# Performance work log

Measured on AMD Instinct MI355X. Metric: run time of the kernel, lower is better.

Reference implementation:

```python
import jax, jax.numpy as jnp
import numpy as np

SHAPES = [(100, 100), (50, 50), (25, 25), (13, 13)]
N_HEADS, N_LEVELS, N_POINTS, D_MODEL, D_FFN = 8, 4, 4, 256, 1024
HEAD_DIM = D_MODEL // N_HEADS
S_TOTAL = sum(h * w for h, w in SHAPES)
BATCH = 2


def _layernorm(x, g, b, eps=1e-5):
    m = jnp.mean(x, -1, keepdims=True)
    v = jnp.mean((x - m) ** 2, -1, keepdims=True)
    return (x - m) * jax.lax.rsqrt(v + eps) * g + b


def _bilinear_sample(value_l, loc, Hl, Wl):
    # value_l: (N, Hl, Wl, nh, hd); loc: (N, Lq, nh, P, 2) normalized to [0,1]
    # Matches torch grid_sample(mode='bilinear', padding_mode='zeros', align_corners=False)
    x = loc[..., 0] * Wl - 0.5
    y = loc[..., 1] * Hl - 0.5
    x0 = jnp.floor(x); y0 = jnp.floor(y)
    wx1 = x - x0; wx0 = 1.0 - wx1
    wy1 = y - y0; wy0 = 1.0 - wy1
    x0i = x0.astype(jnp.int32); x1i = x0i + 1
    y0i = y0.astype(jnp.int32); y1i = y0i + 1
    N, Lq, nh, P = x.shape
    n_idx = jnp.arange(N)[:, None, None, None]
    h_idx = jnp.arange(nh)[None, None, :, None]

    def gather(yi, xi):
        valid = (yi >= 0) & (yi < Hl) & (xi >= 0) & (xi < Wl)
        yc = jnp.clip(yi, 0, Hl - 1); xc = jnp.clip(xi, 0, Wl - 1)
        v = value_l[n_idx, yc, xc, h_idx]  # (N, Lq, nh, P, hd)
        return v * valid[..., None].astype(v.dtype)

    return (gather(y0i, x0i) * (wy0 * wx0)[..., None]
            + gather(y0i, x1i) * (wy0 * wx1)[..., None]
            + gather(y1i, x0i) * (wy1 * wx0)[..., None]
            + gather(y1i, x1i) * (wy1 * wx1)[..., None])


def _forward(src, pos, reference_points, W_off, b_off, W_attn, b_attn, W_val, b_val,
             W_out, b_out, W1, b1, W2, b2, g1, beta1, g2, beta2):
    N, S, C = src.shape
    q = src + pos  # with_pos_embed
    # MSDeformAttn
    off = (q @ W_off + b_off).reshape(N, S, N_HEADS, N_LEVELS, N_POINTS, 2)
    aw = jax.nn.softmax((q @ W_attn + b_attn).reshape(N, S, N_HEADS, N_LEVELS * N_POINTS), axis=-1)
    aw = aw.reshape(N, S, N_HEADS, N_LEVELS, N_POINTS)
    value = (src @ W_val + b_val).reshape(N, S, N_HEADS, HEAD_DIM)
    # offset normalizer is (W_l, H_l) per level
    normalizer = jnp.array([[wl, hl] for hl, wl in SHAPES], dtype=src.dtype)  # (L, 2)
    loc = reference_points[:, :, None, :, None, :] + off / normalizer[None, None, None, :, None, :]
    out = jnp.zeros((N, S, N_HEADS, HEAD_DIM), src.dtype)
    start = 0
    for l, (Hl, Wl) in enumerate(SHAPES):
        v_l = value[:, start:start + Hl * Wl].reshape(N, Hl, Wl, N_HEADS, HEAD_DIM)
        sampled = _bilinear_sample(v_l, loc[:, :, :, l], Hl, Wl)  # (N,S,nh,P,hd)
        out = out + jnp.einsum('nqhp,nqhpd->nqhd', aw[:, :, :, l], sampled)
        start += Hl * Wl
    src2 = out.reshape(N, S, C) @ W_out + b_out
    # residual + norm1 (dropout is identity in eval)
    x = _layernorm(src + src2, g1, beta1)
    # FFN + residual + norm2
    ff = jax.nn.relu(x @ W1 + b1) @ W2 + b2
    return _layernorm(x + ff, g2, beta2)


def setup_inputs() -> dict:
    key = jax.random.key(0)
    ks = jax.random.split(key, 16)
    f32 = jnp.float32

    def w(k, shape, scale=0.02):
        return jax.random.normal(k, shape, dtype=f32) * scale

    return {
        "src": jax.random.normal(ks[0], (BATCH, S_TOTAL, D_MODEL), dtype=f32),
        "pos": jax.random.normal(ks[1], (BATCH, S_TOTAL, D_MODEL), dtype=f32),
        "reference_points": jax.random.uniform(ks[2], (BATCH, S_TOTAL, N_LEVELS, 2), dtype=f32),
        "spatial_shapes": jnp.array(SHAPES, dtype=jnp.int32),
        "level_start_index": jnp.array(np.cumsum([0] + [h * w for h, w in SHAPES[:-1]]), dtype=jnp.int32),
        "W_off": w(ks[3], (D_MODEL, N_HEADS * N_LEVELS * N_POINTS * 2)),
        "b_off": w(ks[4], (N_HEADS * N_LEVELS * N_POINTS * 2,), 0.5),
        "W_attn": w(ks[5], (D_MODEL, N_HEADS * N_LEVELS * N_POINTS)),
        "b_attn": w(ks[6], (N_HEADS * N_LEVELS * N_POINTS,)),
        "W_val": w(ks[7], (D_MODEL, D_MODEL)),
        "b_val": w(ks[8], (D_MODEL,)),
        "W_out": w(ks[9], (D_MODEL, D_MODEL)),
        "b_out": w(ks[10], (D_MODEL,)),
        "W1": w(ks[11], (D_MODEL, D_FFN)),
        "b1": w(ks[12], (D_FFN,)),
        "W2": w(ks[13], (D_FFN, D_MODEL)),
        "b2": w(ks[14], (D_MODEL,)),
        "g1": jnp.ones((D_MODEL,), f32),
        "beta1": jnp.zeros((D_MODEL,), f32),
        "g2": jnp.ones((D_MODEL,), f32),
        "beta2": jnp.zeros((D_MODEL,), f32),
    }


def reference(src, pos, reference_points, spatial_shapes, level_start_index,
              W_off, b_off, W_attn, b_attn, W_val, b_val, W_out, b_out,
              W1, b1, W2, b2, g1, beta1, g2, beta2):
    # spatial_shapes / level_start_index are static metadata mirrored by SHAPES
    return _forward(src, pos, reference_points, W_off, b_off, W_attn, b_attn,
                    W_val, b_val, W_out, b_out, W1, b1, W2, b2, g1, beta1, g2, beta2)
```

## Files before the change

kernel.cpp:

```cpp
#include <hip/hip_runtime.h>


typedef __bf16 bf16x8 __attribute__((ext_vector_type(8)));
typedef __bf16 bf16x4 __attribute__((ext_vector_type(4)));
typedef float floatx4 __attribute__((ext_vector_type(4)));

#define S_TOTAL 13294
#define M_ROWS  26588
#define M_PAD   26624
#define DMODEL  256

struct CvtArgs {
    const float *Woff, *Wattn, *Wval, *Wout, *W1, *W2, *boff, *battn;
};
__global__ __launch_bounds__(256) void cvt_all(CvtArgs a, __bf16* __restrict__ wdst,
                                               float* __restrict__ bc) {
    int i = blockIdx.x * 256 + threadIdx.x;
    if (i < 65536) {
        wdst[i] = (__bf16)a.Woff[(i & 255) * 256 + (i >> 8)];
    } else if (i < 98304) {
        int j = i - 65536;
        wdst[i] = (__bf16)a.Wattn[(j & 255) * 128 + (j >> 8)];
    } else if (i < 163840) {
        int j = i - 98304;
        wdst[i] = (__bf16)a.Wval[(j & 255) * 256 + (j >> 8)];
    } else if (i < 229376) {
        int j = i - 163840;
        wdst[i] = (__bf16)a.Wout[(j & 255) * 256 + (j >> 8)];
    } else if (i < 491520) {
        int j = i - 229376;
        wdst[i] = (__bf16)a.W1[(j & 255) * 1024 + (j >> 8)];
    } else if (i < 753664) {
        int j = i - 491520;
        wdst[i] = (__bf16)a.W2[(j & 1023) * 256 + (j >> 10)];
    } else if (i < 754048) {
        int j = i - 753664;
        bc[j] = (j < 256) ? a.boff[j] : a.battn[j - 256];
    }
}

__global__ __launch_bounds__(256) void prep_k(const float* __restrict__ src,
                                              const float* __restrict__ pos,
                                              __bf16* __restrict__ qb,
                                              __bf16* __restrict__ srcb) {
    int i4 = blockIdx.x * 256 + threadIdx.x;
    size_t e = (size_t)i4 * 4;
    if (e < (size_t)M_ROWS * DMODEL) {
        float4 s = *(const float4*)(src + e);
        float4 p = *(const float4*)(pos + e);
        bf16x4 q = {(__bf16)(s.x + p.x), (__bf16)(s.y + p.y),
                    (__bf16)(s.z + p.z), (__bf16)(s.w + p.w)};
        bf16x4 sb = {(__bf16)s.x, (__bf16)s.y, (__bf16)s.z, (__bf16)s.w};
        *(bf16x4*)(qb + e)   = q;
        *(bf16x4*)(srcb + e) = sb;
    } else {
        bf16x4 z = {(__bf16)0.f, (__bf16)0.f, (__bf16)0.f, (__bf16)0.f};
        *(bf16x4*)(qb + e)   = z;
        *(bf16x4*)(srcb + e) = z;
    }
}

template <int BM, int KT, int J, bool RELU, bool BF16OUT, bool ACCUM>
__global__ __launch_bounds__(512, 4) void gemm_ares(const __bf16* __restrict__ A,
                                                    int lda,
                                                    const __bf16* __restrict__ BT,
                                                    int ldb,
                                                    const float* __restrict__ bias,
                                                    float* __restrict__ Cf,
                                                    __bf16* __restrict__ Cb,
                                                    int N) {
    constexpr int GPR = KT / 8;
    __shared__ __align__(16) __bf16 As[BM * KT];
    __shared__ __align__(16) float  patch[8][16 * 20];

    const int tid  = threadIdx.x;
    const int row0 = blockIdx.y * BM;
    const int wave = tid >> 6, lane = tid & 63;
    const int l16  = lane & 15, quad = lane >> 4;

#pragma unroll
    for (int it = 0; it < BM * GPR / 512; it++) {
        int fg = it * 512 + tid;
        int m  = fg / GPR, g = fg % GPR;
        bf16x8 v = *(const bf16x8*)(A + (size_t)(row0 + m) * lda + g * 8);
        *(bf16x8*)(As + m * KT + (g ^ (m & 31)) * 8) = v;
    }
    __syncthreads();

    const int n0 = blockIdx.x * (8 * J * 16) + wave * (J * 16);
    floatx4 acc[BM / 16][J] = {};

#pragma unroll 4
    for (int ki = 0; ki < KT / 32; ki++) {
        bf16x8 af[BM / 16], bfr[J];
#pragma unroll
        for (int i = 0; i < BM / 16; i++) {
            int row = i * 16 + l16;
            int g   = ki * 4 + quad;
            af[i] = *(const bf16x8*)(As + row * KT + (g ^ (row & 31)) * 8);
        }
#pragma unroll
        for (int j = 0; j < J; j++) {
            int n = n0 + j * 16 + l16;
            bfr[j] = *(const bf16x8*)(BT + (size_t)n * ldb + ki * 32 + quad * 8);
        }
#pragma unroll
        for (int i = 0; i < BM / 16; i++)
#pragma unroll
            for (int j = 0; j < J; j++)
                acc[i][j] = __builtin_amdgcn_mfma_f32_16x16x32_bf16(
                    af[i], bfr[j], acc[i][j], 0, 0, 0);
    }

    float bvj[J];
#pragma unroll
    for (int j = 0; j < J; j++) bvj[j] = bias ? bias[n0 + j * 16 + l16] : 0.f;

    float* pat = patch[wave];
    const int prow = lane >> 2, pc = lane & 3;
#pragma unroll
    for (int i = 0; i < BM / 16; i++)
#pragma unroll
        for (int j = 0; j < J; j++) {
#pragma unroll
            for (int r = 0; r < 4; r++) {
                float v = acc[i][j][r] + bvj[j];
                if (RELU) v = fmaxf(v, 0.f);
                pat[(quad * 4 + r) * 20 + l16] = v;
            }
            float4 v4 = *(float4*)&pat[prow * 20 + pc * 4];
            size_t gi = (size_t)(row0 + i * 16 + prow) * N + n0 + j * 16 + pc * 4;
            if (BF16OUT) {
                bf16x4 ob = {(__bf16)v4.x, (__bf16)v4.y, (__bf16)v4.z, (__bf16)v4.w};
                *(bf16x4*)(Cb + gi) = ob;
            } else if (ACCUM) {
                float4 c4 = *(const float4*)(Cf + gi);
                v4.x += c4.x; v4.y += c4.y; v4.z += c4.z; v4.w += c4.w;
                *(float4*)(Cf + gi) = v4;
            } else {
                *(float4*)(Cf + gi) = v4;
            }
        }
}

__global__ __launch_bounds__(256) void sample_k(const float* __restrict__ offa,
                                                const __bf16* __restrict__ valb,
                                                const float* __restrict__ refp,
                                                __bf16* __restrict__ outb) {
    const int r   = blockIdx.x;
    const int tid = threadIdx.x;
    if (r >= M_ROWS) {
        outb[(size_t)r * 256 + tid] = (__bf16)0.f;
        return;
    }
    __shared__ float2 s_wo[4][128];
    const int n = (r >= S_TOTAL) ? 1 : 0;

    if (tid < 128) {
        const int HLc[4] = {100, 50, 25, 13};
        const int STc[4] = {0, 10000, 12500, 13125};
        int lp = tid & 15, l = lp >> 2;
        float logit = offa[(size_t)r * 384 + 256 + tid];
        float mx = logit;
        mx = fmaxf(mx, __shfl_xor(mx, 1));
        mx = fmaxf(mx, __shfl_xor(mx, 2));
        mx = fmaxf(mx, __shfl_xor(mx, 4));
        mx = fmaxf(mx, __shfl_xor(mx, 8));
        float e = __expf(logit - mx);
        float s = e;
        s += __shfl_xor(s, 1); s += __shfl_xor(s, 2);
        s += __shfl_xor(s, 4); s += __shfl_xor(s, 8);
        float aw = e / s;

        float2 o2 = *(const float2*)(offa + (size_t)r * 384 + tid * 2);
        float rx = refp[((size_t)r * 4 + l) * 2];
        float ry = refp[((size_t)r * 4 + l) * 2 + 1];
        int   Wl = HLc[l];
        float x = rx * (float)Wl + o2.x - 0.5f;
        float y = ry * (float)Wl + o2.y - 0.5f;
        float xf = floorf(x), yf = floorf(y);
        float wx1 = x - xf, wy1 = y - yf;
        float wx0 = 1.f - wx1, wy0 = 1.f - wy1;
        int x0 = (int)xf, y0 = (int)yf;
        int base = n * S_TOTAL + STc[l];
#pragma unroll
        for (int c = 0; c < 4; c++) {
            int yy = y0 + (c >> 1), xx = x0 + (c & 1);
            bool valid = (yy >= 0) & (yy < Wl) & (xx >= 0) & (xx < Wl);
            int yc = min(max(yy, 0), Wl - 1);
            int xc = min(max(xx, 0), Wl - 1);
            float w = ((c >> 1) ? wy1 : wy0) * ((c & 1) ? wx1 : wx0);
            int off = (base + yc * Wl + xc) * 512;
            s_wo[c][tid] = make_float2(valid ? w * aw : 0.f, __int_as_float(off));
        }
    }
    __syncthreads();

    const int h  = tid >> 5;
    const int pg = (tid >> 2) & 7;
    const int cg = tid & 3;
    const char* vbase = (const char*)valb + h * 64 + cg * 16;
    float a[8] = {};
#pragma unroll
    for (int pp = 0; pp < 2; pp++) {
        int idx = h * 16 + pg * 2 + pp;
#pragma unroll
        for (int c = 0; c < 4; c++) {
            float2 wo = s_wo[c][idx];
            float  w  = wo.x;
            bf16x8 v  = *(const bf16x8*)(vbase + __float_as_int(wo.y));
#pragma unroll
            for (int k = 0; k < 8; k++) a[k] += w * (float)v[k];
        }
    }
#pragma unroll
    for (int k = 0; k < 8; k++) {
        a[k] += __shfl_xor(a[k], 4);
        a[k] += __shfl_xor(a[k], 8);
        a[k] += __shfl_xor(a[k], 16);
    }
    if (pg == 0) {
        bf16x8 res;
#pragma unroll
        for (int k = 0; k < 8; k++) res[k] = (__bf16)a[k];
        *(bf16x8*)(outb + (size_t)r * 256 + h * 32 + cg * 8) = res;
    }
}

__global__ __launch_bounds__(64) void ln1_k(const float* __restrict__ src,
                                            const float* __restrict__ src2,
                                            const float* __restrict__ g,
                                            const float* __restrict__ b,
                                            float* __restrict__ x,
                                            __bf16* __restrict__ xb) {
    const int r = blockIdx.x, lane = threadIdx.x;
    if (r >= M_ROWS) {
        bf16x4 z = {(__bf16)0.f, (__bf16)0.f, (__bf16)0.f, (__bf16)0.f};
        *(bf16x4*)(xb + (size_t)r * 256 + lane * 4) = z;
        return;
    }
    size_t base = (size_t)r * 256 + lane * 4;
    float4 a = *(const float4*)(src + base);
    float4 c = *(const float4*)(src2 + base);
    float v0 = a.x + c.x, v1 = a.y + c.y, v2 = a.z + c.z, v3 = a.w + c.w;
    float s  = v0 + v1 + v2 + v3;
    float sq = v0 * v0 + v1 * v1 + v2 * v2 + v3 * v3;
    for (int o = 32; o > 0; o >>= 1) {
        s  += __shfl_xor(s, o);
        sq += __shfl_xor(sq, o);
    }
    float mean = s * (1.f / 256.f);
    float var  = sq * (1.f / 256.f) - mean * mean;
    float rs   = rsqrtf(var + 1e-5f);
    float4 gg = *(const float4*)(g + lane * 4);
    float4 bb = *(const float4*)(b + lane * 4);
    float o0 = (v0 - mean) * rs * gg.x + bb.x;
    float o1 = (v1 - mean) * rs * gg.y + bb.y;
    float o2 = (v2 - mean) * rs * gg.z + bb.z;
    float o3 = (v3 - mean) * rs * gg.w + bb.w;
    *(float4*)(x + base) = make_float4(o0, o1, o2, o3);
    bf16x4 ob = {(__bf16)o0, (__bf16)o1, (__bf16)o2, (__bf16)o3};
    *(bf16x4*)(xb + base) = ob;
}

__global__ __launch_bounds__(64) void ln2_k(const float* __restrict__ t,
                                            const float* __restrict__ g,
                                            const float* __restrict__ b,
                                            float* __restrict__ out) {
    const int r = blockIdx.x, lane = threadIdx.x;
    size_t base = (size_t)r * 256 + lane * 4;
    float4 a = *(const float4*)(t + base);
    float v0 = a.x, v1 = a.y, v2 = a.z, v3 = a.w;
    float s  = v0 + v1 + v2 + v3;
    float sq = v0 * v0 + v1 * v1 + v2 * v2 + v3 * v3;
    for (int o = 32; o > 0; o >>= 1) {
        s  += __shfl_xor(s, o);
        sq += __shfl_xor(sq, o);
    }
    float mean = s * (1.f / 256.f);
    float var  = sq * (1.f / 256.f) - mean * mean;
    float rs   = rsqrtf(var + 1e-5f);
    float4 gg = *(const float4*)(g + lane * 4);
    float4 bb = *(const float4*)(b + lane * 4);
    float4 o4;
    o4.x = (v0 - mean) * rs * gg.x + bb.x;
    o4.y = (v1 - mean) * rs * gg.y + bb.y;
    o4.z = (v2 - mean) * rs * gg.z + bb.z;
    o4.w = (v3 - mean) * rs * gg.w + bb.w;
    *(float4*)(out + base) = o4;
}

extern "C" void kernel_launch(void* const* d_in, const int* in_sizes, int n_in,
                              void* d_out, int out_size, void* d_ws, size_t ws_size,
                              hipStream_t stream) {
    const float* src  = (const float*)d_in[0];
    const float* pos  = (const float*)d_in[1];
    const float* refp = (const float*)d_in[2];
    const float* W_off  = (const float*)d_in[5];
    const float* b_off  = (const float*)d_in[6];
    const float* W_attn = (const float*)d_in[7];
    const float* b_attn = (const float*)d_in[8];
    const float* W_val  = (const float*)d_in[9];
    const float* b_val  = (const float*)d_in[10];
    const float* W_out  = (const float*)d_in[11];
    const float* b_out  = (const float*)d_in[12];
    const float* W1     = (const float*)d_in[13];
    const float* b1     = (const float*)d_in[14];
    const float* W2     = (const float*)d_in[15];
    const float* b2     = (const float*)d_in[16];
    const float* g1     = (const float*)d_in[17];
    const float* beta1  = (const float*)d_in[18];
    const float* g2     = (const float*)d_in[19];
    const float* beta2  = (const float*)d_in[20];
    float* out = (float*)d_out;

    const size_t RB = (size_t)M_PAD * 256 * 2;
    const size_t RF = (size_t)M_PAD * 256 * 4;
    char* ws = (char*)d_ws;
    __bf16* qb   = (__bf16*)(ws);
    __bf16* srcb = (__bf16*)(ws + RB);
    float*  offa = (float*)(ws + 2 * RB);
    __bf16* valb = (__bf16*)(ws + 2 * RB + (size_t)M_PAD * 384 * 4);
    __bf16* outb = qb;
    float*  src2 = (float*)(ws + RB);
    float*  x    = (float*)(ws + RB + RF);
    __bf16* xb   = qb;
    __bf16* hbh  = (__bf16*)(ws + 2 * RB + (size_t)M_PAD * 384 * 4);
    char*   regW = ws + 2 * RB + (size_t)M_PAD * 384 * 4 + (size_t)M_PAD * 512 * 2;

    __bf16* WTcomb = (__bf16*)regW;
    __bf16* WTval  = (__bf16*)(regW + 196608);
    __bf16* WTout  = (__bf16*)(regW + 327680);
    __bf16* WT1    = (__bf16*)(regW + 458752);
    __bf16* WT2    = (__bf16*)(regW + 983040);
    float*  bc     = (float*)(regW + 1507328);

    CvtArgs ca = {W_off, W_attn, W_val, W_out, W1, W2, b_off, b_attn};
    cvt_all<<<(754048 + 255) / 256, 256, 0, stream>>>(ca, WTcomb, bc);

    prep_k<<<M_PAD * 256 / 4 / 256, 256, 0, stream>>>(src, pos, qb, srcb);

    gemm_ares<64, 256, 3, false, false, false><<<dim3(1, 416), 512, 0, stream>>>(
        qb, 256, WTcomb, 256, bc, offa, nullptr, 384);
    gemm_ares<64, 256, 2, false, true, false><<<dim3(1, 416), 512, 0, stream>>>(
        srcb, 256, WTval, 256, b_val, nullptr, valb, 256);

    sample_k<<<M_PAD, 256, 0, stream>>>(offa, valb, refp, outb);

    gemm_ares<64, 256, 2, false, false, false><<<dim3(1, 416), 512, 0, stream>>>(
        outb, 256, WTout, 256, b_out, src2, nullptr, 256);
    ln1_k<<<M_PAD, 64, 0, stream>>>(src, src2, g1, beta1, x, xb);

    for (int half = 0; half < 2; half++) {
        gemm_ares<64, 256, 2, true, true, false><<<dim3(2, 416), 512, 0, stream>>>(
            xb, 256, WT1 + (size_t)half * 512 * 256, 256, b1 + half * 512,
            nullptr, hbh, 512);
        gemm_ares<32, 512, 2, false, false, true><<<dim3(1, 832), 512, 0, stream>>>(
            hbh, 512, WT2 + half * 512, 1024, half == 0 ? b2 : nullptr,
            x, nullptr, 256);
    }
    ln2_k<<<M_ROWS, 64, 0, stream>>>(x, g2, beta2, out);
}
```

Measured before the change: 392.6 us.

## Fuse input prep into GEMMs, output proj with LN1, and full FFN with LN2

Replaces the separate prep, LayerNorm and split FFN kernels with fused kernels. The offset/value GEMMs now read fp32 src/pos directly and convert to bf16 in shared memory. The output projection folds in the residual add and LayerNorm1, and a single FFN kernel keeps the hidden activations in LDS before applying LayerNorm2. The weight-convert kernel now transposes through LDS tiles so its global accesses are coalesced. This removes several intermediate global round-trips and kernel launches, at the cost of more LDS per block and lower parallelism in the fused FFN.

```diff
diff --git a/kernel.cpp b/kernel.cpp
--- a/kernel.cpp
+++ b/kernel.cpp
@@ -8,135 +8,106 @@
 #define S_TOTAL 13294
 #define M_ROWS  26588
 #define M_PAD   26624
-#define DMODEL  256
-
-struct CvtArgs {
-    const float *Woff, *Wattn, *Wval, *Wout, *W1, *W2, *boff, *battn;
-};
-__global__ __launch_bounds__(256) void cvt_all(CvtArgs a, __bf16* __restrict__ wdst,
-                                               float* __restrict__ bc) {
-    int i = blockIdx.x * 256 + threadIdx.x;
-    if (i < 65536) {
-        wdst[i] = (__bf16)a.Woff[(i & 255) * 256 + (i >> 8)];
-    } else if (i < 98304) {
-        int j = i - 65536;
-        wdst[i] = (__bf16)a.Wattn[(j & 255) * 128 + (j >> 8)];
-    } else if (i < 163840) {
-        int j = i - 98304;
-        wdst[i] = (__bf16)a.Wval[(j & 255) * 256 + (j >> 8)];
-    } else if (i < 229376) {
-        int j = i - 163840;
-        wdst[i] = (__bf16)a.Wout[(j & 255) * 256 + (j >> 8)];
-    } else if (i < 491520) {
-        int j = i - 229376;
-        wdst[i] = (__bf16)a.W1[(j & 255) * 1024 + (j >> 8)];
-    } else if (i < 753664) {
-        int j = i - 491520;
-        wdst[i] = (__bf16)a.W2[(j & 1023) * 256 + (j >> 10)];
-    } else if (i < 754048) {
-        int j = i - 753664;
-        bc[j] = (j < 256) ? a.boff[j] : a.battn[j - 256];
-    }
-}
-
-__global__ __launch_bounds__(256) void prep_k(const float* __restrict__ src,
-                                              const float* __restrict__ pos,
-                                              __bf16* __restrict__ qb,
-                                              __bf16* __restrict__ srcb) {
-    int i4 = blockIdx.x * 256 + threadIdx.x;
-    size_t e = (size_t)i4 * 4;
-    if (e < (size_t)M_ROWS * DMODEL) {
-        float4 s = *(const float4*)(src + e);
-        float4 p = *(const float4*)(pos + e);
-        bf16x4 q = {(__bf16)(s.x + p.x), (__bf16)(s.y + p.y),
-                    (__bf16)(s.z + p.z), (__bf16)(s.w + p.w)};
-        bf16x4 sb = {(__bf16)s.x, (__bf16)s.y, (__bf16)s.z, (__bf16)s.w};
-        *(bf16x4*)(qb + e)   = q;
-        *(bf16x4*)(srcb + e) = sb;
-    } else {
-        bf16x4 z = {(__bf16)0.f, (__bf16)0.f, (__bf16)0.f, (__bf16)0.f};
-        *(bf16x4*)(qb + e)   = z;
-        *(bf16x4*)(srcb + e) = z;
-    }
-}
-
-template <int BM, int KT, int J, bool RELU, bool BF16OUT, bool ACCUM>
-__global__ __launch_bounds__(512, 4) void gemm_ares(const __bf16* __restrict__ A,
-                                                    int lda,
-                                                    const __bf16* __restrict__ BT,
-                                                    int ldb,
-                                                    const float* __restrict__ bias,
-                                                    float* __restrict__ Cf,
-                                                    __bf16* __restrict__ Cb,
-                                                    int N) {
-    constexpr int GPR = KT / 8;
-    __shared__ __align__(16) __bf16 As[BM * KT];
-    __shared__ __align__(16) float  patch[8][16 * 20];
-
-    const int tid  = threadIdx.x;
-    const int row0 = blockIdx.y * BM;
-    const int wave = tid >> 6, lane = tid & 63;
-    const int l16  = lane & 15, quad = lane >> 4;
-
-#pragma unroll
-    for (int it = 0; it < BM * GPR / 512; it++) {
-        int fg = it * 512 + tid;
-        int m  = fg / GPR, g = fg % GPR;
-        bf16x8 v = *(const bf16x8*)(A + (size_t)(row0 + m) * lda + g * 8);
-        *(bf16x8*)(As + m * KT + (g ^ (m & 31)) * 8) = v;
-    }
-    __syncthreads();
-
-    const int n0 = blockIdx.x * (8 * J * 16) + wave * (J * 16);
-    floatx4 acc[BM / 16][J] = {};
-
-#pragma unroll 4
-    for (int ki = 0; ki < KT / 32; ki++) {
-        bf16x8 af[BM / 16], bfr[J];
-#pragma unroll
-        for (int i = 0; i < BM / 16; i++) {
-            int row = i * 16 + l16;
-            int g   = ki * 4 + quad;
-            af[i] = *(const bf16x8*)(As + row * KT + (g ^ (row & 31)) * 8);
-        }
-#pragma unroll
-        for (int j = 0; j < J; j++) {
-            int n = n0 + j * 16 + l16;
-            bfr[j] = *(const bf16x8*)(BT + (size_t)n * ldb + ki * 32 + quad * 8);
-        }
-#pragma unroll
-        for (int i = 0; i < BM / 16; i++)
+
+#define MFMA16(a, b, c) __builtin_amdgcn_mfma_f32_16x16x32_bf16(a, b, c, 0, 0, 0)
+
+__global__ __launch_bounds__(256) void cvt_k(
+    const float* __restrict__ Woff, const float* __restrict__ Wattn,
+    const float* __restrict__ Wval, const float* __restrict__ Wout,
+    const float* __restrict__ W1,   const float* __restrict__ W2,
+    const float* __restrict__ boff, const float* __restrict__ battn,
+    __bf16* __restrict__ wbase, float* __restrict__ bc) {
+    int b = blockIdx.x;
+    if (b >= 184) {
+        for (int i = threadIdx.x; i < 384; i += 256)
+            bc[i] = (i < 256) ? boff[i] : battn[i - 256];
+        return;
+    }
+    const float* W; __bf16* D; int K, N, t;
+    if (b < 16)       { W = Woff;  D = wbase;          K = 256;  N = 256;  t = b; }
+    else if (b < 24)  { W = Wattn; D = wbase + 65536;  K = 256;  N = 128;  t = b - 16; }
+    else if (b < 40)  { W = Wval;  D = wbase + 98304;  K = 256;  N = 256;  t = b - 24; }
+    else if (b < 56)  { W = Wout;  D = wbase + 163840; K = 256;  N = 256;  t = b - 40; }
+    else if (b < 120) { W = W1;    D = wbase + 229376; K = 256;  N = 1024; t = b - 56; }
+    else              { W = W2;    D = wbase + 491520; K = 1024; N = 256;  t = b - 120; }
+    int tk = K >> 6;
+    int n0 = (t / tk) << 6, k0 = (t % tk) << 6;
+    __shared__ float T[64][65];
+    int tid = threadIdx.x;
+    int rr = tid >> 4, cc = (tid & 15) << 2;
+#pragma unroll
+    for (int p = 0; p < 4; p++) {
+        int r = p * 16 + rr;
+        float4 v = *(const float4*)(W + (size_t)(k0 + r) * N + n0 + cc);
+        T[r][cc] = v.x; T[r][cc + 1] = v.y; T[r][cc + 2] = v.z; T[r][cc + 3] = v.w;
+    }
+    __syncthreads();
+#pragma unroll
+    for (int p = 0; p < 4; p++) {
+        int n = p * 16 + rr;
+        bf16x4 o = {(__bf16)T[cc][n], (__bf16)T[cc + 1][n],
+                    (__bf16)T[cc + 2][n], (__bf16)T[cc + 3][n]};
+        *(bf16x4*)(D + (size_t)(n0 + n) * K + k0 + cc) = o;
+    }
+}
+
+template <int J, bool SUMPOS, bool BF16OUT>
+__global__ __launch_bounds__(512, 4) void gemm_src(
+    const float* __restrict__ Af, const float* __restrict__ Pf,
+    const __bf16* __restrict__ BT, const float* __restrict__ bias,
+    float* __restrict__ Cf, __bf16* __restrict__ Cb, int N) {
+    constexpr int ASTR = 264;
+    __shared__ __align__(16) __bf16 As[64 * ASTR];
+    __shared__ __align__(16) float patch[8][16 * 20];
+    const int tid = threadIdx.x, wave = tid >> 6, lane = tid & 63;
+    const int l16 = lane & 15, quad = lane >> 4;
+    const int row0 = blockIdx.x * 64;
+#pragma unroll
+    for (int p = 0; p < 8; p++) {
+        int fe = (p * 512 + tid) * 4;
+        int m = fe >> 8, k = fe & 255;
+        int row = min(row0 + m, M_ROWS - 1);
+        float4 s = *(const float4*)(Af + (size_t)row * 256 + k);
+        if (SUMPOS) {
+            float4 pp = *(const float4*)(Pf + (size_t)row * 256 + k);
+            s.x += pp.x; s.y += pp.y; s.z += pp.z; s.w += pp.w;
+        }
+        bf16x4 v = {(__bf16)s.x, (__bf16)s.y, (__bf16)s.z, (__bf16)s.w};
+        *(bf16x4*)(As + m * ASTR + k) = v;
+    }
+    __syncthreads();
+    const int n0 = wave * (J * 16);
+    floatx4 acc[4][J] = {};
+#pragma unroll
+    for (int ki = 0; ki < 8; ki++) {
+        bf16x8 af[4], bfr[J];
+#pragma unroll
+        for (int i = 0; i < 4; i++)
+            af[i] = *(const bf16x8*)(As + (i * 16 + l16) * ASTR + ki * 32 + quad * 8);
+#pragma unroll
+        for (int j = 0; j < J; j++)
+            bfr[j] = *(const bf16x8*)(BT + (size_t)(n0 + j * 16 + l16) * 256 + ki * 32 + quad * 8);
+#pragma unroll
+        for (int i = 0; i < 4; i++)
 #pragma unroll
             for (int j = 0; j < J; j++)
-                acc[i][j] = __builtin_amdgcn_mfma_f32_16x16x32_bf16(
-                    af[i], bfr[j], acc[i][j], 0, 0, 0);
-    }
-
-    float bvj[J];
-#pragma unroll
-    for (int j = 0; j < J; j++) bvj[j] = bias ? bias[n0 + j * 16 + l16] : 0.f;
-
+                acc[i][j] = MFMA16(af[i], bfr[j], acc[i][j]);
+    }
     float* pat = patch[wave];
     const int prow = lane >> 2, pc = lane & 3;
 #pragma unroll
-    for (int i = 0; i < BM / 16; i++)
+    for (int i = 0; i < 4; i++)
 #pragma unroll
         for (int j = 0; j < J; j++) {
-#pragma unroll
-            for (int r = 0; r < 4; r++) {
-                float v = acc[i][j][r] + bvj[j];
-                if (RELU) v = fmaxf(v, 0.f);
-                pat[(quad * 4 + r) * 20 + l16] = v;
-            }
+            float bv = bias[n0 + j * 16 + l16];
+#pragma unroll
+            for (int r = 0; r < 4; r++)
+                pat[(quad * 4 + r) * 20 + l16] = acc[i][j][r] + bv;
             float4 v4 = *(float4*)&pat[prow * 20 + pc * 4];
             size_t gi = (size_t)(row0 + i * 16 + prow) * N + n0 + j * 16 + pc * 4;
             if (BF16OUT) {
                 bf16x4 ob = {(__bf16)v4.x, (__bf16)v4.y, (__bf16)v4.z, (__bf16)v4.w};
                 *(bf16x4*)(Cb + gi) = ob;
-            } else if (ACCUM) {
-                float4 c4 = *(const float4*)(Cf + gi);
-                v4.x += c4.x; v4.y += c4.y; v4.z += c4.z; v4.w += c4.w;
-                *(float4*)(Cf + gi) = v4;
             } else {
                 *(float4*)(Cf + gi) = v4;
             }
@@ -227,67 +198,228 @@
     }
 }
 
-__global__ __launch_bounds__(64) void ln1_k(const float* __restrict__ src,
-                                            const float* __restrict__ src2,
-                                            const float* __restrict__ g,
-                                            const float* __restrict__ b,
-                                            float* __restrict__ x,
-                                            __bf16* __restrict__ xb) {
-    const int r = blockIdx.x, lane = threadIdx.x;
-    if (r >= M_ROWS) {
-        bf16x4 z = {(__bf16)0.f, (__bf16)0.f, (__bf16)0.f, (__bf16)0.f};
-        *(bf16x4*)(xb + (size_t)r * 256 + lane * 4) = z;
-        return;
-    }
-    size_t base = (size_t)r * 256 + lane * 4;
-    float4 a = *(const float4*)(src + base);
-    float4 c = *(const float4*)(src2 + base);
-    float v0 = a.x + c.x, v1 = a.y + c.y, v2 = a.z + c.z, v3 = a.w + c.w;
-    float s  = v0 + v1 + v2 + v3;
-    float sq = v0 * v0 + v1 * v1 + v2 * v2 + v3 * v3;
-    for (int o = 32; o > 0; o >>= 1) {
-        s  += __shfl_xor(s, o);
-        sq += __shfl_xor(sq, o);
-    }
-    float mean = s * (1.f / 256.f);
-    float var  = sq * (1.f / 256.f) - mean * mean;
-    float rs   = rsqrtf(var + 1e-5f);
-    float4 gg = *(const float4*)(g + lane * 4);
-    float4 bb = *(const float4*)(b + lane * 4);
-    float o0 = (v0 - mean) * rs * gg.x + bb.x;
-    float o1 = (v1 - mean) * rs * gg.y + bb.y;
-    float o2 = (v2 - mean) * rs * gg.z + bb.z;
-    float o3 = (v3 - mean) * rs * gg.w + bb.w;
-    *(float4*)(x + base) = make_float4(o0, o1, o2, o3);
-    bf16x4 ob = {(__bf16)o0, (__bf16)o1, (__bf16)o2, (__bf16)o3};
-    *(bf16x4*)(xb + base) = ob;
-}
-
-__global__ __launch_bounds__(64) void ln2_k(const float* __restrict__ t,
-                                            const float* __restrict__ g,
-                                            const float* __restrict__ b,
-                                            float* __restrict__ out) {
-    const int r = blockIdx.x, lane = threadIdx.x;
-    size_t base = (size_t)r * 256 + lane * 4;
-    float4 a = *(const float4*)(t + base);
-    float v0 = a.x, v1 = a.y, v2 = a.z, v3 = a.w;
-    float s  = v0 + v1 + v2 + v3;
-    float sq = v0 * v0 + v1 * v1 + v2 * v2 + v3 * v3;
-    for (int o = 32; o > 0; o >>= 1) {
-        s  += __shfl_xor(s, o);
-        sq += __shfl_xor(sq, o);
-    }
-    float mean = s * (1.f / 256.f);
-    float var  = sq * (1.f / 256.f) - mean * mean;
-    float rs   = rsqrtf(var + 1e-5f);
-    float4 gg = *(const float4*)(g + lane * 4);
-    float4 bb = *(const float4*)(b + lane * 4);
-    float4 o4;
-    o4.x = (v0 - mean) * rs * gg.x + bb.x;
-    o4.y = (v1 - mean) * rs * gg.y + bb.y;
-    o4.z = (v2 - mean) * rs * gg.z + bb.z;
-    o4.w = (v3 - mean) * rs * gg.w + bb.w;
-    *(float4*)(out + base) = o4;
+__global__ __launch_bounds__(512, 4) void oln_k(
+    const __bf16* __restrict__ A, const __bf16* __restrict__ BT,
+    const float* __restrict__ bias, const float* __restrict__ src,
+    const float* __restrict__ g, const float* __restrict__ be,
+    float* __restrict__ x, __bf16* __restrict__ xb) {
+    constexpr int ASTR = 264;
+    __shared__ __align__(16) __bf16 As[64 * ASTR];
+    __shared__ __align__(16) float patch[8][16 * 20];
+    __shared__ float2 rowred[64][9];
+    const int tid = threadIdx.x, wave = tid >> 6, lane = tid & 63;
+    const int l16 = lane & 15, quad = lane >> 4;
+    const int prow = lane >> 2, pc = lane & 3;
+    const int row0 = blockIdx.x * 64;
+#pragma unroll
+    for (int p = 0; p < 4; p++) {
+        int fg = p * 512 + tid;
+        int m = fg >> 5, gg = fg & 31;
+        bf16x8 v = *(const bf16x8*)(A + (size_t)(row0 + m) * 256 + gg * 8);
+        *(bf16x8*)(As + m * ASTR + gg * 8) = v;
+    }
+    __syncthreads();
+    const int n0 = wave * 32;
+    floatx4 acc[4][2] = {};
+#pragma unroll
+    for (int ki = 0; ki < 8; ki++) {
+        bf16x8 af[4], bfr[2];
+#pragma unroll
+        for (int i = 0; i < 4; i++)
+            af[i] = *(const bf16x8*)(As + (i * 16 + l16) * ASTR + ki * 32 + quad * 8);
+#pragma unroll
+        for (int j = 0; j < 2; j++)
+            bfr[j] = *(const bf16x8*)(BT + (size_t)(n0 + j * 16 + l16) * 256 + ki * 32 + quad * 8);
+#pragma unroll
+        for (int i = 0; i < 4; i++)
+#pragma unroll
+            for (int j = 0; j < 2; j++)
+                acc[i][j] = MFMA16(af[i], bfr[j], acc[i][j]);
+    }
+    float* pat = patch[wave];
+    floatx4 v4[4][2];
+#pragma unroll
+    for (int i = 0; i < 4; i++) {
+        int rowc = min(row0 + i * 16 + prow, M_ROWS - 1);
+        float s_par = 0.f, q_par = 0.f;
+#pragma unroll
+        for (int j = 0; j < 2; j++) {
+            float bv = bias[n0 + j * 16 + l16];
+#pragma unroll
+            for (int r = 0; r < 4; r++)
+                pat[(quad * 4 + r) * 20 + l16] = acc[i][j][r] + bv;
+            float4 t4 = *(float4*)&pat[prow * 20 + pc * 4];
+            float4 r4 = *(const float4*)(src + (size_t)rowc * 256 + n0 + j * 16 + pc * 4);
+            floatx4 w; w[0] = t4.x + r4.x; w[1] = t4.y + r4.y;
+            w[2] = t4.z + r4.z; w[3] = t4.w + r4.w;
+            v4[i][j] = w;
+            s_par += w[0] + w[1] + w[2] + w[3];
+            q_par += w[0] * w[0] + w[1] * w[1] + w[2] * w[2] + w[3] * w[3];
+        }
+        s_par += __shfl_xor(s_par, 1); s_par += __shfl_xor(s_par, 2);
+        q_par += __shfl_xor(q_par, 1); q_par += __shfl_xor(q_par, 2);
+        if (pc == 0) rowred[i * 16 + prow][wave] = make_float2(s_par, q_par);
+    }
+    __syncthreads();
+#pragma unroll
+    for (int i = 0; i < 4; i++) {
+        float ss = 0.f, qq = 0.f;
+#pragma unroll
+        for (int w8 = 0; w8 < 8; w8++) {
+            float2 t = rowred[i * 16 + prow][w8];
+            ss += t.x; qq += t.y;
+        }
+        float mean = ss * (1.f / 256.f);
+        float var  = qq * (1.f / 256.f) - mean * mean;
+        float rstd = rsqrtf(var + 1e-5f);
+#pragma unroll
+        for (int j = 0; j < 2; j++) {
+            int col = n0 + j * 16 + pc * 4;
+            float4 g4 = *(const float4*)(g + col);
+            float4 b4 = *(const float4*)(be + col);
+            floatx4 w = v4[i][j];
+            float4 o4;
+            o4.x = (w[0] - mean) * rstd * g4.x + b4.x;
+            o4.y = (w[1] - mean) * rstd * g4.y + b4.y;
+            o4.z = (w[2] - mean) * rstd * g4.z + b4.z;
+            o4.w = (w[3] - mean) * rstd * g4.w + b4.w;
+            size_t gi = (size_t)(row0 + i * 16 + prow) * 256 + col;
+            *(float4*)(x + gi) = o4;
+            bf16x4 ob = {(__bf16)o4.x, (__bf16)o4.y, (__bf16)o4.z, (__bf16)o4.w};
+            *(bf16x4*)(xb + gi) = ob;
+        }
+    }
+}
+
+__global__ __launch_bounds__(512, 4) void ffn_k(
+    const __bf16* __restrict__ xb, const __bf16* __restrict__ W1T,
+    const __bf16* __restrict__ W2T, const float* __restrict__ b1,
+    const float* __restrict__ b2, const float* __restrict__ x,
+    const float* __restrict__ g, const float* __restrict__ be,
+    float* __restrict__ out) {
+    constexpr int ASTR = 264, HSTR = 520;
+    __shared__ __align__(16) __bf16 As[32 * ASTR];
+    __shared__ __align__(16) __bf16 Hs[32 * HSTR];
+    __shared__ __align__(16) float patch[8][16 * 20];
+    __shared__ float2 rowred[32][9];
+    const int tid = threadIdx.x, wave = tid >> 6, lane = tid & 63;
+    const int l16 = lane & 15, quad = lane >> 4;
+    const int prow = lane >> 2, pc = lane & 3;
+    const int row0 = blockIdx.x * 32;
+    float* pat = patch[wave];
+#pragma unroll
+    for (int p = 0; p < 2; p++) {
+        int fg = p * 512 + tid;
+        int m = fg >> 5, gg = fg & 31;
+        bf16x8 v = *(const bf16x8*)(xb + (size_t)(row0 + m) * 256 + gg * 8);
+        *(bf16x8*)(As + m * ASTR + gg * 8) = v;
+    }
+    __syncthreads();
+    floatx4 facc[2][2] = {};
+    for (int hc = 0; hc < 2; hc++) {
+        floatx4 hacc[2][4] = {};
+#pragma unroll
+        for (int ki = 0; ki < 8; ki++) {
+            bf16x8 af[2], bfr[4];
+#pragma unroll
+            for (int i = 0; i < 2; i++)
+                af[i] = *(const bf16x8*)(As + (i * 16 + l16) * ASTR + ki * 32 + quad * 8);
+#pragma unroll
+            for (int j = 0; j < 4; j++) {
+                int nn = hc * 512 + wave * 64 + j * 16 + l16;
+                bfr[j] = *(const bf16x8*)(W1T + (size_t)nn * 256 + ki * 32 + quad * 8);
+            }
+#pragma unroll
+            for (int i = 0; i < 2; i++)
+#pragma unroll
+                for (int j = 0; j < 4; j++)
+                    hacc[i][j] = MFMA16(af[i], bfr[j], hacc[i][j]);
+        }
+#pragma unroll
+        for (int i = 0; i < 2; i++)
+#pragma unroll
+            for (int j = 0; j < 4; j++) {
+                float bv = b1[hc * 512 + wave * 64 + j * 16 + l16];
+#pragma unroll
+                for (int r = 0; r < 4; r++)
+                    pat[(quad * 4 + r) * 20 + l16] = fmaxf(hacc[i][j][r] + bv, 0.f);
+                float4 t4 = *(float4*)&pat[prow * 20 + pc * 4];
+                bf16x4 h4 = {(__bf16)t4.x, (__bf16)t4.y, (__bf16)t4.z, (__bf16)t4.w};
+                *(bf16x4*)(Hs + (i * 16 + prow) * HSTR + wave * 64 + j * 16 + pc * 4) = h4;
+            }
+        __syncthreads();
+#pragma unroll
+        for (int ki = 0; ki < 16; ki++) {
+            bf16x8 ah[2], bfr[2];
+#pragma unroll
+            for (int i = 0; i < 2; i++)
+                ah[i] = *(const bf16x8*)(Hs + (i * 16 + l16) * HSTR + ki * 32 + quad * 8);
+#pragma unroll
+            for (int j = 0; j < 2; j++) {
+                int nn = wave * 32 + j * 16 + l16;
+                bfr[j] = *(const bf16x8*)(W2T + (size_t)nn * 1024 + hc * 512 + ki * 32 + quad * 8);
+            }
+#pragma unroll
+            for (int i = 0; i < 2; i++)
+#pragma unroll
+                for (int j = 0; j < 2; j++)
+                    facc[i][j] = MFMA16(ah[i], bfr[j], facc[i][j]);
+        }
+        __syncthreads();
+    }
+    const int n0 = wave * 32;
+    floatx4 v4[2][2];
+#pragma unroll
+    for (int i = 0; i < 2; i++) {
+        int rowi = row0 + i * 16 + prow;
+        float s_par = 0.f, q_par = 0.f;
+#pragma unroll
+        for (int j = 0; j < 2; j++) {
+            float bv = b2[n0 + j * 16 + l16];
+#pragma unroll
+            for (int r = 0; r < 4; r++)
+                pat[(quad * 4 + r) * 20 + l16] = facc[i][j][r] + bv;
+            float4 t4 = *(float4*)&pat[prow * 20 + pc * 4];
+            float4 r4 = *(const float4*)(x + (size_t)rowi * 256 + n0 + j * 16 + pc * 4);
+            floatx4 w; w[0] = t4.x + r4.x; w[1] = t4.y + r4.y;
+            w[2] = t4.z + r4.z; w[3] = t4.w + r4.w;
+            v4[i][j] = w;
+            s_par += w[0] + w[1] + w[2] + w[3];
+            q_par += w[0] * w[0] + w[1] * w[1] + w[2] * w[2] + w[3] * w[3];
+        }
+        s_par += __shfl_xor(s_par, 1); s_par += __shfl_xor(s_par, 2);
+        q_par += __shfl_xor(q_par, 1); q_par += __shfl_xor(q_par, 2);
+        if (pc == 0) rowred[i * 16 + prow][wave] = make_float2(s_par, q_par);
+    }
+    __syncthreads();
+#pragma unroll
+    for (int i = 0; i < 2; i++) {
+        float ss = 0.f, qq = 0.f;
+#pragma unroll
+        for (int w8 = 0; w8 < 8; w8++) {
+            float2 t = rowred[i * 16 + prow][w8];
+            ss += t.x; qq += t.y;
+        }
+        float mean = ss * (1.f / 256.f);
+        float var  = qq * (1.f / 256.f) - mean * mean;
+        float rstd = rsqrtf(var + 1e-5f);
+        int row = row0 + i * 16 + prow;
+        if (row < M_ROWS) {
+#pragma unroll
+            for (int j = 0; j < 2; j++) {
+                int col = n0 + j * 16 + pc * 4;
+                float4 g4 = *(const float4*)(g + col);
+                float4 b4 = *(const float4*)(be + col);
+                floatx4 w = v4[i][j];
+                float4 o4;
+                o4.x = (w[0] - mean) * rstd * g4.x + b4.x;
+                o4.y = (w[1] - mean) * rstd * g4.y + b4.y;
+                o4.z = (w[2] - mean) * rstd * g4.z + b4.z;
+                o4.w = (w[3] - mean) * rstd * g4.w + b4.w;
+                *(float4*)(out + (size_t)row * 256 + col) = o4;
+            }
+        }
+    }
 }
 
 extern "C" void kernel_launch(void* const* d_in, const int* in_sizes, int n_in,
@@ -317,16 +449,12 @@
     const size_t RB = (size_t)M_PAD * 256 * 2;
     const size_t RF = (size_t)M_PAD * 256 * 4;
     char* ws = (char*)d_ws;
-    __bf16* qb   = (__bf16*)(ws);
-    __bf16* srcb = (__bf16*)(ws + RB);
+    __bf16* outb = (__bf16*)(ws);
+    __bf16* valb = (__bf16*)(ws + RB);
     float*  offa = (float*)(ws + 2 * RB);
-    __bf16* valb = (__bf16*)(ws + 2 * RB + (size_t)M_PAD * 384 * 4);
-    __bf16* outb = qb;
-    float*  src2 = (float*)(ws + RB);
-    float*  x    = (float*)(ws + RB + RF);
-    __bf16* xb   = qb;
-    __bf16* hbh  = (__bf16*)(ws + 2 * RB + (size_t)M_PAD * 384 * 4);
-    char*   regW = ws + 2 * RB + (size_t)M_PAD * 384 * 4 + (size_t)M_PAD * 512 * 2;
+    float*  x    = (float*)(ws + 2 * RB);
+    __bf16* xb   = (__bf16*)(ws + 2 * RB + RF);
+    char*   regW = ws + 2 * RB + (size_t)M_PAD * 384 * 4;
 
     __bf16* WTcomb = (__bf16*)regW;
     __bf16* WTval  = (__bf16*)(regW + 196608);
@@ -335,29 +463,17 @@
     __bf16* WT2    = (__bf16*)(regW + 983040);
     float*  bc     = (float*)(regW + 1507328);
 
-    CvtArgs ca = {W_off, W_attn, W_val, W_out, W1, W2, b_off, b_attn};
-    cvt_all<<<(754048 + 255) / 256, 256, 0, stream>>>(ca, WTcomb, bc);
-
-    prep_k<<<M_PAD * 256 / 4 / 256, 256, 0, stream>>>(src, pos, qb, srcb);
-
-    gemm_ares<64, 256, 3, false, false, false><<<dim3(1, 416), 512, 0, stream>>>(
-        qb, 256, WTcomb, 256, bc, offa, nullptr, 384);
-    gemm_ares<64, 256, 2, false, true, false><<<dim3(1, 416), 512, 0, stream>>>(
-        srcb, 256, WTval, 256, b_val, nullptr, valb, 256);
+    cvt_k<<<185, 256, 0, stream>>>(W_off, W_attn, W_val, W_out, W1, W2,
+                                   b_off, b_attn, WTcomb, bc);
+
+    gemm_src<3, true, false><<<416, 512, 0, stream>>>(
+        src, pos, WTcomb, bc, offa, nullptr, 384);
+    gemm_src<2, false, true><<<416, 512, 0, stream>>>(
+        src, src, WTval, b_val, nullptr, valb, 256);
 
     sample_k<<<M_PAD, 256, 0, stream>>>(offa, valb, refp, outb);
 
-    gemm_ares<64, 256, 2, false, false, false><<<dim3(1, 416), 512, 0, stream>>>(
-        outb, 256, WTout, 256, b_out, src2, nullptr, 256);
-    ln1_k<<<M_PAD, 64, 0, stream>>>(src, src2, g1, beta1, x, xb);
-
-    for (int half = 0; half < 2; half++) {
-        gemm_ares<64, 256, 2, true, true, false><<<dim3(2, 416), 512, 0, stream>>>(
-            xb, 256, WT1 + (size_t)half * 512 * 256, 256, b1 + half * 512,
-            nullptr, hbh, 512);
-        gemm_ares<32, 512, 2, false, false, true><<<dim3(1, 832), 512, 0, stream>>>(
-            hbh, 512, WT2 + half * 512, 1024, half == 0 ? b2 : nullptr,
-            x, nullptr, 256);
-    }
-    ln2_k<<<M_ROWS, 64, 0, stream>>>(x, g2, beta2, out);
-}
+    oln_k<<<416, 512, 0, stream>>>(outb, WTout, b_out, src, g1, beta1, x, xb);
+
+    ffn_k<<<832, 512, 0, stream>>>(xb, WT1, WT2, b1, b2, x, g2, beta2, out);
+}
```

New measurement: 362.7 us. -7.6%, faster.
